# Kernel tuning notes

Measured on AMD Instinct MI355X. Metric: run time of the kernel, lower is better.

Reference implementation:

```python
import jax, jax.numpy as jnp
import numpy as np

B, C_IMG, H, W = 64, 256, 64, 64
HID, T = 512, 128
M, A = 128, 128  # multifeat_size, attfeat_size


def setup_inputs() -> dict:
    key = jax.random.key(0)
    ks = jax.random.split(key, 9)
    s = 0.02
    return {
        "img_feat": jax.random.normal(ks[0], (B, C_IMG, H, W), jnp.float32),
        "text_feat": jax.random.normal(ks[1], (B, HID, T), jnp.float32),
        "W_img": jax.random.normal(ks[2], (M, C_IMG), jnp.float32) * s,   # in_img_conv 1x1
        "W_txt": jax.random.normal(ks[3], (M, HID), jnp.float32) * s,     # in_text_conv 1d k=1
        "W_qfc": jax.random.normal(ks[4], (A, M), jnp.float32) * s,       # multi_qfc
        "W_ifc": jax.random.normal(ks[5], (A, M), jnp.float32) * s,       # multi_ifc
        "W_ipc": jax.random.normal(ks[6], (A, M), jnp.float32) * s,       # ifeat_proj_conv 1x1
        "W_qpc": jax.random.normal(ks[7], (A, M), jnp.float32) * s,       # qfeat_proj_conv 1x1
        "W_att": jax.random.normal(ks[8], (1, A), jnp.float32) * s,       # att_conv 1x1
    }


def reference(img_feat, text_feat, W_img, W_txt, W_qfc, W_ifc, W_ipc, W_qpc, W_att):
    b, c, h, w = img_feat.shape
    n = h * w  # conv_feat_num
    x = img_feat.reshape(b, c, n)
    # in_img_conv: dropout(id) -> 1x1 conv -> tanh ; in_text_conv analogous
    in_ifeat = jnp.tanh(jnp.einsum("mc,bcn->bmn", W_img, x))        # [B,M,HW]
    in_qfeat = jnp.tanh(jnp.einsum("mh,bht->bmt", W_txt, text_feat))  # [B,M,T]

    # text-guided image attention branch
    qfeatatt = jnp.mean(in_qfeat, axis=2) @ W_qfc.T                  # [B,A]
    ifeatproj = jnp.einsum("am,bmn->ban", W_ipc, in_ifeat)           # [B,A,HW]
    addfeat_i = jnp.tanh(qfeatatt[:, :, None] + ifeatproj)

    # image-guided text attention branch
    ifeatatt = jnp.mean(in_ifeat, axis=2) @ W_ifc.T                  # [B,A]
    qfeatproj = jnp.einsum("am,bmt->bat", W_qpc, in_qfeat)           # [B,A,T]
    addfeat_q = jnp.tanh(ifeatatt[:, :, None] + qfeatproj)

    attfeat_join = jnp.concatenate([addfeat_i, addfeat_q], axis=2)   # [B,A,HW+T]
    att_logits = jnp.einsum("a,ban->bn", W_att[0], attfeat_join)     # [B,HW+T]
    att = jax.nn.softmax(att_logits, axis=1)

    joint_feat = jnp.concatenate([in_ifeat, in_qfeat], axis=2)       # [B,M,HW+T]
    att_feat = jnp.einsum("bmn,bn->bm", joint_feat, att)             # [B,M]
    return att_feat, att
```

## Files before the change

### kernel.cpp

```cpp
#include <hip/hip_runtime.h>
#include <hip/hip_bf16.h>

#define DI static __device__ __forceinline__

typedef unsigned short u16;
typedef unsigned int   u32;
typedef __bf16 bf16_t;
typedef __bf16 bf16x8 __attribute__((ext_vector_type(8)));
typedef float  f32x4  __attribute__((ext_vector_type(4)));

union BF8 { ushort4 u4[2]; bf16x8 v; };

DI u16 f2bf(float f) { union { bf16_t b; u16 u; } c; c.b = (bf16_t)f; return c.u; }
DI float bf2f(u32 lo) { union { u32 u; float f; } c; c.u = lo << 16; return c.f; }
DI float fast_tanh(float x) { float e = __expf(2.0f * x); return 1.0f - 2.0f / (e + 1.0f); }

constexpr int NB   = 64;
constexpr int HW   = 4096;
constexpr int TT   = 128;
constexpr int NTOT = HW + TT;

constexpr size_t WS_WIMG  = 0;
constexpr size_t WS_WTXT  = WS_WIMG  + 128ull*256*2;
constexpr size_t WS_WIPC  = WS_WTXT  + 128ull*512*2;
constexpr size_t WS_WQPC  = WS_WIPC  + 128ull*128*2;
constexpr size_t WS_IFEAT = WS_WQPC  + 128ull*128*2;
constexpr size_t WS_QFEAT = WS_IFEAT + (size_t)NB*128*HW*2;
constexpr size_t WS_QFP   = WS_QFEAT + (size_t)NB*128*TT*2;
constexpr size_t WS_LOGIT = WS_QFP   + (size_t)NB*128*TT*4;
constexpr size_t WS_ISUM  = WS_LOGIT + (size_t)NB*NTOT*4;
constexpr size_t WS_QSUM  = WS_ISUM  + (size_t)NB*128*4;
constexpr size_t WS_QATT  = WS_QSUM  + (size_t)NB*128*4;

__global__ void k_zero(float* __restrict__ p, int n) {
    int i = blockIdx.x * 256 + threadIdx.x;
    if (i < n) p[i] = 0.0f;
}

__global__ void k_convert4(const float* __restrict__ s0, const float* __restrict__ s1,
                           const float* __restrict__ s2, const float* __restrict__ s3,
                           bf16_t* __restrict__ d0, bf16_t* __restrict__ d1,
                           bf16_t* __restrict__ d2, bf16_t* __restrict__ d3) {
    int i = blockIdx.x * 256 + threadIdx.x;
    if (i < 32768) { d0[i] = (bf16_t)s0[i]; return; }
    i -= 32768;
    if (i < 65536) { d1[i] = (bf16_t)s1[i]; return; }
    i -= 65536;
    if (i < 16384) { d2[i] = (bf16_t)s2[i]; return; }
    i -= 16384;
    d3[i] = (bf16_t)s3[i];
}

__global__ void k_qatt(const float* __restrict__ qsum, const float* __restrict__ Wqfc,
                       float* __restrict__ qatt) {
    int b = blockIdx.x, a = threadIdx.x;
    const float* qs = qsum + b * 128;
    const float* wr = Wqfc + a * 128;
    float s = 0.f;
    for (int m = 0; m < 128; ++m) s += qs[m] * wr[m];
    qatt[b * 128 + a] = s * (1.0f / 128.0f);
}

__global__ void k_textlogits(const float* __restrict__ isum, const float* __restrict__ Wifc,
                             const float* __restrict__ Watt, const float* __restrict__ qfp,
                             float* __restrict__ logits) {
    int b = blockIdx.x, tid = threadIdx.x;
    __shared__ float ia[128];
    __shared__ float wat[128];
    __shared__ float part[2][128];
    if (tid < 128) {
        float s = 0.f;
        const float* is = isum + b * 128;
        const float* wr = Wifc + tid * 128;
        for (int m = 0; m < 128; ++m) s += is[m] * wr[m];
        ia[tid]  = s * (1.0f / 4096.0f);
        wat[tid] = Watt[tid];
    }
    __syncthreads();
    int t = tid & 127, h = tid >> 7;
    const float* qp = qfp + ((size_t)b * 128 + h * 64) * 128 + t;
    float s = 0.f;
    for (int a0 = 0; a0 < 64; ++a0) {
        int a = h * 64 + a0;
        s += wat[a] * fast_tanh(ia[a] + qp[(size_t)a0 * 128]);
    }
    part[h][t] = s;
    __syncthreads();
    if (tid < 128) logits[b * NTOT + 4096 + tid] = part[0][tid] + part[1][tid];
}

__global__ void k_softmax(const float* __restrict__ logits, float* __restrict__ att) {
    int b = blockIdx.x, tid = threadIdx.x;
    const float* L = logits + (size_t)b * NTOT;
    float* O = att + (size_t)b * NTOT;
    __shared__ float red[4];
    __shared__ float red2[4];
    float mx = -3.0e38f;
    for (int i = tid; i < NTOT; i += 256) mx = fmaxf(mx, L[i]);
    for (int off = 1; off < 64; off <<= 1) mx = fmaxf(mx, __shfl_xor(mx, off, 64));
    if ((tid & 63) == 0) red[tid >> 6] = mx;
    __syncthreads();
    mx = fmaxf(fmaxf(red[0], red[1]), fmaxf(red[2], red[3]));
    float s = 0.f;
    for (int i = tid; i < NTOT; i += 256) {
        float e = __expf(L[i] - mx);
        O[i] = e;
        s += e;
    }
    for (int off = 1; off < 64; off <<= 1) s += __shfl_xor(s, off, 64);
    if ((tid & 63) == 0) red2[tid >> 6] = s;
    __syncthreads();
    float inv = 1.0f / (red2[0] + red2[1] + red2[2] + red2[3]);
    for (int i = tid; i < NTOT; i += 256) O[i] *= inv;
}

__global__ void k_attfeat(const bf16_t* __restrict__ ifeat, const bf16_t* __restrict__ qfeat,
                          const float* __restrict__ att, float* __restrict__ out) {
    int mg = blockIdx.x;
    int ns = blockIdx.y;
    int b  = blockIdx.z;
    int tid = threadIdx.x;
    const u16* F = (const u16*)ifeat + ((size_t)b * 128 + mg * 8) * HW;
    const u16* Q = (const u16*)qfeat + ((size_t)b * 128 + mg * 8) * TT;
    const float* A_ = att + (size_t)b * NTOT;
    float acc[8] = {0, 0, 0, 0, 0, 0, 0, 0};
    int i0 = ns * 512;
#pragma unroll
    for (int it = 0; it < 2; ++it) {
        int i = i0 + it * 256 + tid;
        float2 a2 = *(const float2*)&A_[2 * i];
#pragma unroll
        for (int r = 0; r < 8; ++r) {
            u32 pk = *(const u32*)&F[(size_t)r * HW + 2 * i];
            acc[r] += bf2f(pk & 0xffffu) * a2.x + bf2f(pk >> 16) * a2.y;
        }
    }
    if (ns == 0 && tid < TT / 2) {
        float2 a2 = *(const float2*)&A_[HW + 2 * tid];
#pragma unroll
        for (int r = 0; r < 8; ++r) {
            u32 pk = *(const u32*)&Q[(size_t)r * TT + 2 * tid];
            acc[r] += bf2f(pk & 0xffffu) * a2.x + bf2f(pk >> 16) * a2.y;
        }
    }
    __shared__ float red[4][8];
    int lane = tid & 63, wv = tid >> 6;
#pragma unroll
    for (int r = 0; r < 8; ++r) {
        float s = acc[r];
        s += __shfl_xor(s, 1, 64);
        s += __shfl_xor(s, 2, 64);
        s += __shfl_xor(s, 4, 64);
        s += __shfl_xor(s, 8, 64);
        s += __shfl_xor(s, 16, 64);
        s += __shfl_xor(s, 32, 64);
        if (lane == 0) red[wv][r] = s;
    }
    __syncthreads();
    if (tid < 8)
        atomicAdd(&out[(size_t)b * 128 + mg * 8 + tid],
                  red[0][tid] + red[1][tid] + red[2][tid] + red[3][tid]);
}

template <int C, bool IMG>
__global__ __launch_bounds__(256, 4) void k_chain(
    const float* __restrict__ xin, const bf16_t* __restrict__ Wa, const bf16_t* __restrict__ Wp,
    const float* __restrict__ qatt, const float* __restrict__ Watt, bf16_t* __restrict__ feat_out,
    float* __restrict__ sums, float* __restrict__ proj_out, int S) {
    constexpr int NCH = C / 128;
    __shared__ u16 XY[128 * 68];
    __shared__ u16 Y1[64 * 132];
    __shared__ float lred[4][64];
    __shared__ float qf_l[128];
    __shared__ float wa_l[128];

    const int tid = threadIdx.x;
    const int b  = blockIdx.y;
    const int n0 = blockIdx.x * 64;
    const int l  = tid & 63, w = tid >> 6;
    const int lr = l & 15, g = l >> 4;

    if constexpr (IMG) {
        if (tid < 128) {
            qf_l[tid] = qatt[b * 128 + tid];
            wa_l[tid] = Watt[tid];
        }
    }

    f32x4 acc1[2][4];
#pragma unroll
    for (int rt = 0; rt < 2; ++rt)
#pragma unroll
        for (int ct = 0; ct < 4; ++ct)
#pragma unroll
            for (int r = 0; r < 4; ++r) acc1[rt][ct][r] = 0.f;

    const bf16_t* wa0 = Wa + (size_t)(w * 32 + lr) * C + g * 8;
    const int colb = (tid & 15) * 4;
    const int r0   = tid >> 4;

    for (int h = 0; h < NCH; ++h) {
        {
            const float* xb = xin + (size_t)b * C * S + (size_t)h * 128 * S + n0 + colb;
#pragma unroll
            for (int p = 0; p < 8; ++p) {
                int c2 = p * 16 + r0;
                float4 f = *(const float4*)(xb + (size_t)c2 * S);
                u16 v[4] = {f2bf(f.x), f2bf(f.y), f2bf(f.z), f2bf(f.w)};
                int rot = c2 & 3;
#pragma unroll
                for (int s = 0; s < 4; ++s) {
                    int jj = (s + rot) & 3;
                    XY[(colb + jj) * 132 + c2] = v[jj];
                }
            }
        }
        __syncthreads();
#pragma unroll
        for (int ks2 = 0; ks2 < 4; ++ks2) {
            int ks = h * 4 + ks2;
            bf16x8 af0 = *(const bf16x8*)(wa0 + ks * 32);
            bf16x8 af1 = *(const bf16x8*)(wa0 + (size_t)16 * C + ks * 32);
#pragma unroll
            for (int ct = 0; ct < 4; ++ct) {
                BF8 bu;
                const u16* p = &XY[(ct * 16 + lr) * 132 + ks2 * 32 + g * 8];
                bu.u4[0] = *(const ushort4*)p;
                bu.u4[1] = *(const ushort4*)(p + 4);
                acc1[0][ct] = __builtin_amdgcn_mfma_f32_16x16x32_bf16(af0, bu.v, acc1[0][ct], 0, 0, 0);
                acc1[1][ct] = __builtin_amdgcn_mfma_f32_16x16x32_bf16(af1, bu.v, acc1[1][ct], 0, 0, 0);
            }
        }
        __syncthreads();
    }

    float y[2][4][4];
#pragma unroll
    for (int rt = 0; rt < 2; ++rt)
#pragma unroll
        for (int ct = 0; ct < 4; ++ct)
#pragma unroll
            for (int r = 0; r < 4; ++r) y[rt][ct][r] = fast_tanh(acc1[rt][ct][r]);

#pragma unroll
    for (int rt = 0; rt < 2; ++rt)
#pragma unroll
        for (int r = 0; r < 4; ++r) {
            float s = y[rt][0][r] + y[rt][1][r] + y[rt][2][r] + y[rt][3][r];
            s += __shfl_xor(s, 1, 64);
            s += __shfl_xor(s, 2, 64);
            s += __shfl_xor(s, 4, 64);
            s += __shfl_xor(s, 8, 64);
            if (lr == 0) atomicAdd(&sums[b * 128 + w * 32 + rt * 16 + g * 4 + r], s);
        }

#pragma unroll
    for (int rt = 0; rt < 2; ++rt)
#pragma unroll
        for (int ct = 0; ct < 4; ++ct) {
            int m0 = w * 32 + rt * 16 + g * 4;
            int c2 = ct * 16 + lr;
#pragma unroll
            for (int r = 0; r < 4; r += 2) {
                u32 pk = (u32)f2bf(y[rt][ct][r]) | ((u32)f2bf(y[rt][ct][r + 1]) << 16);
                *(u32*)&Y1[c2 * 132 + m0 + r] = pk;
            }
#pragma unroll
            for (int r = 0; r < 4; ++r) XY[(m0 + r) * 68 + c2] = f2bf(y[rt][ct][r]);
        }
    __syncthreads();

    f32x4 acc2[2][4];
#pragma unroll
    for (int rt = 0; rt < 2; ++rt)
#pragma unroll
        for (int ct = 0; ct < 4; ++ct)
#pragma unroll
            for (int r = 0; r < 4; ++r) acc2[rt][ct][r] = 0.f;

    const bf16_t* wp0 = Wp + (size_t)(w * 32 + lr) * 128 + g * 8;
#pragma unroll
    for (int ks = 0; ks < 4; ++ks) {
        bf16x8 af0 = *(const bf16x8*)(wp0 + ks * 32);
        bf16x8 af1 = *(const bf16x8*)(wp0 + 16 * 128 + ks * 32);
#pragma unroll
        for (int ct = 0; ct < 4; ++ct) {
            BF8 bu;
            const u16* p = &Y1[(ct * 16 + lr) * 132 + ks * 32 + g * 8];
            bu.u4[0] = *(const ushort4*)p;
            bu.u4[1] = *(const ushort4*)(p + 4);
            acc2[0][ct] = __builtin_amdgcn_mfma_f32_16x16x32_bf16(af0, bu.v, acc2[0][ct], 0, 0, 0);
            acc2[1][ct] = __builtin_amdgcn_mfma_f32_16x16x32_bf16(af1, bu.v, acc2[1][ct], 0, 0, 0);
        }
    }

    {
        u16* fb = (u16*)feat_out + (size_t)b * 128 * S + n0;
#pragma unroll
        for (int it = 0; it < 8; ++it) {
            int m = w * 32 + it * 4 + g;
            int nc = lr * 4;
            ushort4 v = *(const ushort4*)&XY[m * 68 + nc];
            *(ushort4*)(fb + (size_t)m * S + nc) = v;
        }
    }

    if constexpr (IMG) {
        float ps[4] = {0, 0, 0, 0};
#pragma unroll
        for (int rt = 0; rt < 2; ++rt)
#pragma unroll
            for (int r = 0; r < 4; ++r) {
                int a = w * 32 + rt * 16 + g * 4 + r;
                float qa = qf_l[a], wv = wa_l[a];
#pragma unroll
                for (int ct = 0; ct < 4; ++ct) ps[ct] += wv * fast_tanh(qa + acc2[rt][ct][r]);
            }
#pragma unroll
        for (int ct = 0; ct < 4; ++ct) {
            ps[ct] += __shfl_xor(ps[ct], 16, 64);
            ps[ct] += __shfl_xor(ps[ct], 32, 64);
        }
        if (g == 0) {
#pragma unroll
            for (int ct = 0; ct < 4; ++ct) lred[w][ct * 16 + lr] = ps[ct];
        }
        __syncthreads();
        if (tid < 64)
            proj_out[(size_t)b * NTOT + n0 + tid] =
                lred[0][tid] + lred[1][tid] + lred[2][tid] + lred[3][tid];
    } else {
#pragma unroll
        for (int rt = 0; rt < 2; ++rt)
#pragma unroll
            for (int ct = 0; ct < 4; ++ct) {
                int a = w * 32 + rt * 16 + g * 4;
                int t = n0 + ct * 16 + lr;
#pragma unroll
                for (int r = 0; r < 4; ++r)
                    proj_out[((size_t)b * 128 + a + r) * 128 + t] = acc2[rt][ct][r];
            }
    }
}

extern "C" void kernel_launch(void* const* d_in, const int* in_sizes, int n_in, void* d_out,
                              int out_size, void* d_ws, size_t ws_size, hipStream_t stream) {
    (void)in_sizes; (void)n_in; (void)out_size; (void)ws_size;
    const float* img  = (const float*)d_in[0];
    const float* txt  = (const float*)d_in[1];
    const float* Wimg = (const float*)d_in[2];
    const float* Wtxt = (const float*)d_in[3];
    const float* Wqfc = (const float*)d_in[4];
    const float* Wifc = (const float*)d_in[5];
    const float* Wipc = (const float*)d_in[6];
    const float* Wqpc = (const float*)d_in[7];
    const float* Watt = (const float*)d_in[8];

    char* ws = (char*)d_ws;
    bf16_t* wimg_b  = (bf16_t*)(ws + WS_WIMG);
    bf16_t* wtxt_b  = (bf16_t*)(ws + WS_WTXT);
    bf16_t* wipc_b  = (bf16_t*)(ws + WS_WIPC);
    bf16_t* wqpc_b  = (bf16_t*)(ws + WS_WQPC);
    bf16_t* ifeat_b = (bf16_t*)(ws + WS_IFEAT);
    bf16_t* qfeat_b = (bf16_t*)(ws + WS_QFEAT);
    float*  qfp     = (float*)(ws + WS_QFP);
    float*  logits  = (float*)(ws + WS_LOGIT);
    float*  isum    = (float*)(ws + WS_ISUM);
    float*  qsum    = (float*)(ws + WS_QSUM);
    float*  qatt    = (float*)(ws + WS_QATT);

    float* out_feat = (float*)d_out;
    float* out_att  = (float*)d_out + 64 * 128;

    k_zero<<<(2 * 64 * 128 + 255) / 256, 256, 0, stream>>>(isum, 2 * 64 * 128);
    k_zero<<<(64 * 128 + 255) / 256, 256, 0, stream>>>(out_feat, 64 * 128);

    k_convert4<<<131072 / 256, 256, 0, stream>>>(Wimg, Wtxt, Wipc, Wqpc,
                                                 wimg_b, wtxt_b, wipc_b, wqpc_b);

    k_chain<512, false><<<dim3(2, 64), 256, 0, stream>>>(txt, wtxt_b, wqpc_b, nullptr, nullptr,
                                                         qfeat_b, qsum, qfp, TT);
    k_qatt<<<64, 128, 0, stream>>>(qsum, Wqfc, qatt);
    k_chain<256, true><<<dim3(64, 64), 256, 0, stream>>>(img, wimg_b, wipc_b, qatt, Watt,
                                                         ifeat_b, isum, logits, HW);
    k_textlogits<<<64, 256, 0, stream>>>(isum, Wifc, Watt, qfp, logits);
    k_softmax<<<64, 256, 0, stream>>>(logits, out_att);
    k_attfeat<<<dim3(16, 4, 64), 256, 0, stream>>>(ifeat_b, qfeat_b, out_att, out_feat);
}
```

Baseline: 491.8 us.

## Fuse small kernels, double-buffer chain loads, vectorize attfeat reduction

Merges the zero and weight-convert launches into one init kernel. Folds the qatt matvec into the image chain kernel and combines text logits with the softmax in one kernel that keeps logits in shared memory. The chain kernel now prefetches 64-channel chunks into double-buffered LDS so global loads overlap the MFMA work. The attfeat kernel switches to 16-byte bf16 loads with four rows per half-block. Together these cut launch count and global round trips, at the cost of recomputing qatt in every image block.

```diff
diff --git a/kernel.cpp b/kernel.cpp
--- a/kernel.cpp
+++ b/kernel.cpp
@@ -28,90 +28,291 @@
 constexpr size_t WS_QFEAT = WS_IFEAT + (size_t)NB*128*HW*2;
 constexpr size_t WS_QFP   = WS_QFEAT + (size_t)NB*128*TT*2;
 constexpr size_t WS_LOGIT = WS_QFP   + (size_t)NB*128*TT*4;
-constexpr size_t WS_ISUM  = WS_LOGIT + (size_t)NB*NTOT*4;
+constexpr size_t WS_ISUM  = WS_LOGIT + (size_t)NB*HW*4;
 constexpr size_t WS_QSUM  = WS_ISUM  + (size_t)NB*128*4;
-constexpr size_t WS_QATT  = WS_QSUM  + (size_t)NB*128*4;
-
-__global__ void k_zero(float* __restrict__ p, int n) {
+
+__global__ void k_init(const float* __restrict__ s0, const float* __restrict__ s1,
+                       const float* __restrict__ s2, const float* __restrict__ s3,
+                       bf16_t* __restrict__ d0, bf16_t* __restrict__ d1,
+                       bf16_t* __restrict__ d2, bf16_t* __restrict__ d3,
+                       float* __restrict__ sums, float* __restrict__ outf) {
     int i = blockIdx.x * 256 + threadIdx.x;
-    if (i < n) p[i] = 0.0f;
+    if (i < 16384) sums[i] = 0.f;
+    else if (i < 24576) outf[i - 16384] = 0.f;
+    int j = i;
+    if (j < 32768) { d0[j] = (bf16_t)s0[j]; return; }
+    j -= 32768;
+    if (j < 65536) { d1[j] = (bf16_t)s1[j]; return; }
+    j -= 65536;
+    if (j < 16384) { d2[j] = (bf16_t)s2[j]; return; }
+    j -= 16384;
+    d3[j] = (bf16_t)s3[j];
 }
 
-__global__ void k_convert4(const float* __restrict__ s0, const float* __restrict__ s1,
-                           const float* __restrict__ s2, const float* __restrict__ s3,
-                           bf16_t* __restrict__ d0, bf16_t* __restrict__ d1,
-                           bf16_t* __restrict__ d2, bf16_t* __restrict__ d3) {
-    int i = blockIdx.x * 256 + threadIdx.x;
-    if (i < 32768) { d0[i] = (bf16_t)s0[i]; return; }
-    i -= 32768;
-    if (i < 65536) { d1[i] = (bf16_t)s1[i]; return; }
-    i -= 65536;
-    if (i < 16384) { d2[i] = (bf16_t)s2[i]; return; }
-    i -= 16384;
-    d3[i] = (bf16_t)s3[i];
+template <int C, bool IMG>
+__global__ __launch_bounds__(256, 4) void k_chain(
+    const float* __restrict__ xin, const bf16_t* __restrict__ Wa, const bf16_t* __restrict__ Wp,
+    const float* __restrict__ qsum, const float* __restrict__ Wqfc, const float* __restrict__ Watt,
+    bf16_t* __restrict__ feat_out, float* __restrict__ sums, float* __restrict__ proj_out, int S) {
+    constexpr int NCH = C / 64;
+    __shared__ u16 XY[2][64 * 68];
+    __shared__ u16 Y1[64 * 132];
+    __shared__ float lred[4][64];
+    __shared__ float qf_l[128];
+    __shared__ float wa_l[128];
+
+    const int tid = threadIdx.x;
+    const int b  = blockIdx.y;
+    const int n0 = blockIdx.x * 64;
+    const int l  = tid & 63, w = tid >> 6;
+    const int lr = l & 15, g = l >> 4;
+
+    f32x4 acc1[2][4];
+#pragma unroll
+    for (int rt = 0; rt < 2; ++rt)
+#pragma unroll
+        for (int ct = 0; ct < 4; ++ct)
+#pragma unroll
+            for (int r = 0; r < 4; ++r) acc1[rt][ct][r] = 0.f;
+
+    const bf16_t* wa0 = Wa + (size_t)(w * 32 + lr) * C + g * 8;
+    const int colb = (tid & 15) * 4;
+    const int rb   = tid >> 4;
+    const float* xbase = xin + (size_t)b * C * S + n0 + colb;
+    float4 pf[4];
+
+#pragma unroll
+    for (int p = 0; p < 4; ++p) pf[p] = *(const float4*)(xbase + (size_t)(rb + p * 16) * S);
+#pragma unroll
+    for (int p = 0; p < 4; ++p) {
+        int c2 = rb + p * 16;
+        u16 v[4] = {f2bf(pf[p].x), f2bf(pf[p].y), f2bf(pf[p].z), f2bf(pf[p].w)};
+        int rot = c2 & 3;
+#pragma unroll
+        for (int s = 0; s < 4; ++s) { int jj = (s + rot) & 3; XY[0][(colb + jj) * 68 + c2] = v[jj]; }
+    }
+
+    for (int h = 0; h < NCH; ++h) {
+        __syncthreads();
+        if (h + 1 < NCH) {
+            const float* xb = xbase + (size_t)((h + 1) * 64) * S;
+#pragma unroll
+            for (int p = 0; p < 4; ++p) pf[p] = *(const float4*)(xb + (size_t)(rb + p * 16) * S);
+        }
+#pragma unroll
+        for (int ks2 = 0; ks2 < 2; ++ks2) {
+            int ks = h * 2 + ks2;
+            bf16x8 af0 = *(const bf16x8*)(wa0 + ks * 32);
+            bf16x8 af1 = *(const bf16x8*)(wa0 + (size_t)16 * C + ks * 32);
+#pragma unroll
+            for (int ct = 0; ct < 4; ++ct) {
+                BF8 bu;
+                const u16* p = &XY[h & 1][(ct * 16 + lr) * 68 + ks2 * 32 + g * 8];
+                bu.u4[0] = *(const ushort4*)p;
+                bu.u4[1] = *(const ushort4*)(p + 4);
+                acc1[0][ct] = __builtin_amdgcn_mfma_f32_16x16x32_bf16(af0, bu.v, acc1[0][ct], 0, 0, 0);
+                acc1[1][ct] = __builtin_amdgcn_mfma_f32_16x16x32_bf16(af1, bu.v, acc1[1][ct], 0, 0, 0);
+            }
+        }
+        if (h + 1 < NCH) {
+#pragma unroll
+            for (int p = 0; p < 4; ++p) {
+                int c2 = rb + p * 16;
+                u16 v[4] = {f2bf(pf[p].x), f2bf(pf[p].y), f2bf(pf[p].z), f2bf(pf[p].w)};
+                int rot = c2 & 3;
+#pragma unroll
+                for (int s = 0; s < 4; ++s) {
+                    int jj = (s + rot) & 3;
+                    XY[(h + 1) & 1][(colb + jj) * 68 + c2] = v[jj];
+                }
+            }
+        }
+    }
+    __syncthreads();
+
+#pragma unroll
+    for (int rt = 0; rt < 2; ++rt)
+#pragma unroll
+        for (int ct = 0; ct < 4; ++ct)
+#pragma unroll
+            for (int r = 0; r < 4; ++r) acc1[rt][ct][r] = fast_tanh(acc1[rt][ct][r]);
+
+#pragma unroll
+    for (int rt = 0; rt < 2; ++rt)
+#pragma unroll
+        for (int r = 0; r < 4; ++r) {
+            float s = acc1[rt][0][r] + acc1[rt][1][r] + acc1[rt][2][r] + acc1[rt][3][r];
+            s += __shfl_xor(s, 1, 64);
+            s += __shfl_xor(s, 2, 64);
+            s += __shfl_xor(s, 4, 64);
+            s += __shfl_xor(s, 8, 64);
+            if (lr == 0) atomicAdd(&sums[b * 128 + w * 32 + rt * 16 + g * 4 + r], s);
+        }
+
+    u16* Y1N = &XY[0][0];
+#pragma unroll
+    for (int rt = 0; rt < 2; ++rt)
+#pragma unroll
+        for (int ct = 0; ct < 4; ++ct) {
+            int m0 = w * 32 + rt * 16 + g * 4;
+            int c2 = ct * 16 + lr;
+#pragma unroll
+            for (int r = 0; r < 4; r += 2) {
+                u32 pk = (u32)f2bf(acc1[rt][ct][r]) | ((u32)f2bf(acc1[rt][ct][r + 1]) << 16);
+                *(u32*)&Y1[c2 * 132 + m0 + r] = pk;
+            }
+#pragma unroll
+            for (int r = 0; r < 4; ++r) Y1N[(m0 + r) * 68 + c2] = f2bf(acc1[rt][ct][r]);
+        }
+    __syncthreads();
+
+    if constexpr (IMG) {
+        if (tid < 128) {
+            const float4* qs4 = (const float4*)(qsum + b * 128);
+            const float4* wr4 = (const float4*)(Wqfc + (size_t)tid * 128);
+            float s = 0.f;
+#pragma unroll 8
+            for (int m = 0; m < 32; ++m) {
+                float4 a = qs4[m], c = wr4[m];
+                s += a.x * c.x + a.y * c.y + a.z * c.z + a.w * c.w;
+            }
+            qf_l[tid] = s * (1.0f / 128.0f);
+            wa_l[tid] = Watt[tid];
+        }
+    }
+
+    f32x4 acc2[2][4];
+#pragma unroll
+    for (int rt = 0; rt < 2; ++rt)
+#pragma unroll
+        for (int ct = 0; ct < 4; ++ct)
+#pragma unroll
+            for (int r = 0; r < 4; ++r) acc2[rt][ct][r] = 0.f;
+
+    const bf16_t* wp0 = Wp + (size_t)(w * 32 + lr) * 128 + g * 8;
+#pragma unroll
+    for (int ks = 0; ks < 4; ++ks) {
+        bf16x8 af0 = *(const bf16x8*)(wp0 + ks * 32);
+        bf16x8 af1 = *(const bf16x8*)(wp0 + 16 * 128 + ks * 32);
+#pragma unroll
+        for (int ct = 0; ct < 4; ++ct) {
+            BF8 bu;
+            const u16* p = &Y1[(ct * 16 + lr) * 132 + ks * 32 + g * 8];
+            bu.u4[0] = *(const ushort4*)p;
+            bu.u4[1] = *(const ushort4*)(p + 4);
+            acc2[0][ct] = __builtin_amdgcn_mfma_f32_16x16x32_bf16(af0, bu.v, acc2[0][ct], 0, 0, 0);
+            acc2[1][ct] = __builtin_amdgcn_mfma_f32_16x16x32_bf16(af1, bu.v, acc2[1][ct], 0, 0, 0);
+        }
+    }
+
+    {
+        u16* fb = (u16*)feat_out + (size_t)b * 128 * S + n0;
+#pragma unroll
+        for (int it = 0; it < 8; ++it) {
+            int m = w * 32 + it * 4 + g;
+            int nc = lr * 4;
+            ushort4 v = *(const ushort4*)&Y1N[m * 68 + nc];
+            *(ushort4*)(fb + (size_t)m * S + nc) = v;
+        }
+    }
+
+    if constexpr (IMG) {
+        __syncthreads();
+        float ps[4] = {0, 0, 0, 0};
+#pragma unroll
+        for (int rt = 0; rt < 2; ++rt)
+#pragma unroll
+            for (int r = 0; r < 4; ++r) {
+                int a = w * 32 + rt * 16 + g * 4 + r;
+                float qa = qf_l[a], wv = wa_l[a];
+#pragma unroll
+                for (int ct = 0; ct < 4; ++ct) ps[ct] += wv * fast_tanh(qa + acc2[rt][ct][r]);
+            }
+#pragma unroll
+        for (int ct = 0; ct < 4; ++ct) {
+            ps[ct] += __shfl_xor(ps[ct], 16, 64);
+            ps[ct] += __shfl_xor(ps[ct], 32, 64);
+        }
+        if (g == 0) {
+#pragma unroll
+            for (int ct = 0; ct < 4; ++ct) lred[w][ct * 16 + lr] = ps[ct];
+        }
+        __syncthreads();
+        if (tid < 64)
+            proj_out[(size_t)b * HW + n0 + tid] =
+                lred[0][tid] + lred[1][tid] + lred[2][tid] + lred[3][tid];
+    } else {
+#pragma unroll
+        for (int rt = 0; rt < 2; ++rt)
+#pragma unroll
+            for (int ct = 0; ct < 4; ++ct) {
+                int a = w * 32 + rt * 16 + g * 4;
+                int t = n0 + ct * 16 + lr;
+#pragma unroll
+                for (int r = 0; r < 4; ++r)
+                    proj_out[((size_t)b * 128 + a + r) * 128 + t] = acc2[rt][ct][r];
+            }
+    }
 }
 
-__global__ void k_qatt(const float* __restrict__ qsum, const float* __restrict__ Wqfc,
-                       float* __restrict__ qatt) {
-    int b = blockIdx.x, a = threadIdx.x;
-    const float* qs = qsum + b * 128;
-    const float* wr = Wqfc + a * 128;
-    float s = 0.f;
-    for (int m = 0; m < 128; ++m) s += qs[m] * wr[m];
-    qatt[b * 128 + a] = s * (1.0f / 128.0f);
-}
-
-__global__ void k_textlogits(const float* __restrict__ isum, const float* __restrict__ Wifc,
-                             const float* __restrict__ Watt, const float* __restrict__ qfp,
-                             float* __restrict__ logits) {
+__global__ void k_finish(const float* __restrict__ isum, const float* __restrict__ Wifc,
+                         const float* __restrict__ Watt, const float* __restrict__ qfp,
+                         const float* __restrict__ logitsI, float* __restrict__ att) {
     int b = blockIdx.x, tid = threadIdx.x;
+    __shared__ float L[NTOT];
     __shared__ float ia[128];
     __shared__ float wat[128];
     __shared__ float part[2][128];
+    __shared__ float redm[4];
+    __shared__ float reds[4];
+
     if (tid < 128) {
+        const float4* is4 = (const float4*)(isum + b * 128);
+        const float4* wr4 = (const float4*)(Wifc + (size_t)tid * 128);
         float s = 0.f;
-        const float* is = isum + b * 128;
-        const float* wr = Wifc + tid * 128;
-        for (int m = 0; m < 128; ++m) s += is[m] * wr[m];
+#pragma unroll 8
+        for (int m = 0; m < 32; ++m) {
+            float4 a = is4[m], c = wr4[m];
+            s += a.x * c.x + a.y * c.y + a.z * c.z + a.w * c.w;
+        }
         ia[tid]  = s * (1.0f / 4096.0f);
         wat[tid] = Watt[tid];
     }
-    __syncthreads();
-    int t = tid & 127, h = tid >> 7;
-    const float* qp = qfp + ((size_t)b * 128 + h * 64) * 128 + t;
-    float s = 0.f;
-    for (int a0 = 0; a0 < 64; ++a0) {
-        int a = h * 64 + a0;
-        s += wat[a] * fast_tanh(ia[a] + qp[(size_t)a0 * 128]);
-    }
-    part[h][t] = s;
-    __syncthreads();
-    if (tid < 128) logits[b * NTOT + 4096 + tid] = part[0][tid] + part[1][tid];
-}
-
-__global__ void k_softmax(const float* __restrict__ logits, float* __restrict__ att) {
-    int b = blockIdx.x, tid = threadIdx.x;
-    const float* L = logits + (size_t)b * NTOT;
+    const float4* LI = (const float4*)(logitsI + (size_t)b * HW);
+#pragma unroll
+    for (int i = 0; i < 4; ++i) *(float4*)&L[(i * 256 + tid) * 4] = LI[i * 256 + tid];
+    __syncthreads();
+
+    {
+        int t = tid & 127, h = tid >> 7;
+        const float* qp = qfp + ((size_t)b * 128 + h * 64) * 128 + t;
+        float s = 0.f;
+        for (int a0 = 0; a0 < 64; ++a0)
+            s += wat[h * 64 + a0] * fast_tanh(ia[h * 64 + a0] + qp[(size_t)a0 * 128]);
+        part[h][t] = s;
+    }
+    __syncthreads();
+    if (tid < 128) L[HW + tid] = part[0][tid] + part[1][tid];
+    __syncthreads();
+
     float* O = att + (size_t)b * NTOT;
-    __shared__ float red[4];
-    __shared__ float red2[4];
     float mx = -3.0e38f;
     for (int i = tid; i < NTOT; i += 256) mx = fmaxf(mx, L[i]);
     for (int off = 1; off < 64; off <<= 1) mx = fmaxf(mx, __shfl_xor(mx, off, 64));
-    if ((tid & 63) == 0) red[tid >> 6] = mx;
-    __syncthreads();
-    mx = fmaxf(fmaxf(red[0], red[1]), fmaxf(red[2], red[3]));
+    if ((tid & 63) == 0) redm[tid >> 6] = mx;
+    __syncthreads();
+    mx = fmaxf(fmaxf(redm[0], redm[1]), fmaxf(redm[2], redm[3]));
     float s = 0.f;
     for (int i = tid; i < NTOT; i += 256) {
         float e = __expf(L[i] - mx);
-        O[i] = e;
+        L[i] = e;
         s += e;
     }
     for (int off = 1; off < 64; off <<= 1) s += __shfl_xor(s, off, 64);
-    if ((tid & 63) == 0) red2[tid >> 6] = s;
-    __syncthreads();
-    float inv = 1.0f / (red2[0] + red2[1] + red2[2] + red2[3]);
-    for (int i = tid; i < NTOT; i += 256) O[i] *= inv;
+    if ((tid & 63) == 0) reds[tid >> 6] = s;
+    __syncthreads();
+    float inv = 1.0f / (reds[0] + reds[1] + reds[2] + reds[3]);
+    for (int i = tid; i < NTOT; i += 256) O[i] = L[i] * inv;
 }
 
 __global__ void k_attfeat(const bf16_t* __restrict__ ifeat, const bf16_t* __restrict__ qfeat,
@@ -120,33 +321,48 @@
     int ns = blockIdx.y;
     int b  = blockIdx.z;
     int tid = threadIdx.x;
-    const u16* F = (const u16*)ifeat + ((size_t)b * 128 + mg * 8) * HW;
-    const u16* Q = (const u16*)qfeat + ((size_t)b * 128 + mg * 8) * TT;
+    int half = tid >> 7;
+    int q = tid & 127;
+    int cx = q * 8;
     const float* A_ = att + (size_t)b * NTOT;
-    float acc[8] = {0, 0, 0, 0, 0, 0, 0, 0};
-    int i0 = ns * 512;
-#pragma unroll
-    for (int it = 0; it < 2; ++it) {
-        int i = i0 + it * 256 + tid;
-        float2 a2 = *(const float2*)&A_[2 * i];
-#pragma unroll
-        for (int r = 0; r < 8; ++r) {
-            u32 pk = *(const u32*)&F[(size_t)r * HW + 2 * i];
-            acc[r] += bf2f(pk & 0xffffu) * a2.x + bf2f(pk >> 16) * a2.y;
-        }
-    }
-    if (ns == 0 && tid < TT / 2) {
-        float2 a2 = *(const float2*)&A_[HW + 2 * tid];
-#pragma unroll
-        for (int r = 0; r < 8; ++r) {
-            u32 pk = *(const u32*)&Q[(size_t)r * TT + 2 * tid];
-            acc[r] += bf2f(pk & 0xffffu) * a2.x + bf2f(pk >> 16) * a2.y;
-        }
-    }
-    __shared__ float red[4][8];
+    const u16* F = (const u16*)ifeat + ((size_t)b * 128 + mg * 8 + half * 4) * HW + ns * 1024 + cx;
+
+    float a8[8];
+    {
+        float4 a0 = *(const float4*)&A_[ns * 1024 + cx];
+        float4 a1 = *(const float4*)&A_[ns * 1024 + cx + 4];
+        a8[0] = a0.x; a8[1] = a0.y; a8[2] = a0.z; a8[3] = a0.w;
+        a8[4] = a1.x; a8[5] = a1.y; a8[6] = a1.z; a8[7] = a1.w;
+    }
+    float acc[4] = {0, 0, 0, 0};
+#pragma unroll
+    for (int r = 0; r < 4; ++r) {
+        uint4 pk = *(const uint4*)&F[(size_t)r * HW];
+        acc[r] += bf2f(pk.x & 0xffffu) * a8[0] + bf2f(pk.x >> 16) * a8[1]
+                + bf2f(pk.y & 0xffffu) * a8[2] + bf2f(pk.y >> 16) * a8[3]
+                + bf2f(pk.z & 0xffffu) * a8[4] + bf2f(pk.z >> 16) * a8[5]
+                + bf2f(pk.w & 0xffffu) * a8[6] + bf2f(pk.w >> 16) * a8[7];
+    }
+    if (ns == 0 && q < 16) {
+        const u16* Q = (const u16*)qfeat + ((size_t)b * 128 + mg * 8 + half * 4) * TT + cx;
+        float b8[8];
+        float4 a0 = *(const float4*)&A_[HW + cx];
+        float4 a1 = *(const float4*)&A_[HW + cx + 4];
+        b8[0] = a0.x; b8[1] = a0.y; b8[2] = a0.z; b8[3] = a0.w;
+        b8[4] = a1.x; b8[5] = a1.y; b8[6] = a1.z; b8[7] = a1.w;
+#pragma unroll
+        for (int r = 0; r < 4; ++r) {
+            uint4 pk = *(const uint4*)&Q[(size_t)r * TT];
+            acc[r] += bf2f(pk.x & 0xffffu) * b8[0] + bf2f(pk.x >> 16) * b8[1]
+                    + bf2f(pk.y & 0xffffu) * b8[2] + bf2f(pk.y >> 16) * b8[3]
+                    + bf2f(pk.z & 0xffffu) * b8[4] + bf2f(pk.z >> 16) * b8[5]
+                    + bf2f(pk.w & 0xffffu) * b8[6] + bf2f(pk.w >> 16) * b8[7];
+        }
+    }
+    __shared__ float red[4][4];
     int lane = tid & 63, wv = tid >> 6;
 #pragma unroll
-    for (int r = 0; r < 8; ++r) {
+    for (int r = 0; r < 4; ++r) {
         float s = acc[r];
         s += __shfl_xor(s, 1, 64);
         s += __shfl_xor(s, 2, 64);
@@ -157,189 +373,10 @@
         if (lane == 0) red[wv][r] = s;
     }
     __syncthreads();
-    if (tid < 8)
-        atomicAdd(&out[(size_t)b * 128 + mg * 8 + tid],
-                  red[0][tid] + red[1][tid] + red[2][tid] + red[3][tid]);
-}
-
-template <int C, bool IMG>
-__global__ __launch_bounds__(256, 4) void k_chain(
-    const float* __restrict__ xin, const bf16_t* __restrict__ Wa, const bf16_t* __restrict__ Wp,
-    const float* __restrict__ qatt, const float* __restrict__ Watt, bf16_t* __restrict__ feat_out,
-    float* __restrict__ sums, float* __restrict__ proj_out, int S) {
-    constexpr int NCH = C / 128;
-    __shared__ u16 XY[128 * 68];
-    __shared__ u16 Y1[64 * 132];
-    __shared__ float lred[4][64];
-    __shared__ float qf_l[128];
-    __shared__ float wa_l[128];
-
-    const int tid = threadIdx.x;
-    const int b  = blockIdx.y;
-    const int n0 = blockIdx.x * 64;
-    const int l  = tid & 63, w = tid >> 6;
-    const int lr = l & 15, g = l >> 4;
-
-    if constexpr (IMG) {
-        if (tid < 128) {
-            qf_l[tid] = qatt[b * 128 + tid];
-            wa_l[tid] = Watt[tid];
-        }
-    }
-
-    f32x4 acc1[2][4];
-#pragma unroll
-    for (int rt = 0; rt < 2; ++rt)
-#pragma unroll
-        for (int ct = 0; ct < 4; ++ct)
-#pragma unroll
-            for (int r = 0; r < 4; ++r) acc1[rt][ct][r] = 0.f;
-
-    const bf16_t* wa0 = Wa + (size_t)(w * 32 + lr) * C + g * 8;
-    const int colb = (tid & 15) * 4;
-    const int r0   = tid >> 4;
-
-    for (int h = 0; h < NCH; ++h) {
-        {
-            const float* xb = xin + (size_t)b * C * S + (size_t)h * 128 * S + n0 + colb;
-#pragma unroll
-            for (int p = 0; p < 8; ++p) {
-                int c2 = p * 16 + r0;
-                float4 f = *(const float4*)(xb + (size_t)c2 * S);
-                u16 v[4] = {f2bf(f.x), f2bf(f.y), f2bf(f.z), f2bf(f.w)};
-                int rot = c2 & 3;
-#pragma unroll
-                for (int s = 0; s < 4; ++s) {
-                    int jj = (s + rot) & 3;
-                    XY[(colb + jj) * 132 + c2] = v[jj];
-                }
-            }
-        }
-        __syncthreads();
-#pragma unroll
-        for (int ks2 = 0; ks2 < 4; ++ks2) {
-            int ks = h * 4 + ks2;
-            bf16x8 af0 = *(const bf16x8*)(wa0 + ks * 32);
-            bf16x8 af1 = *(const bf16x8*)(wa0 + (size_t)16 * C + ks * 32);
-#pragma unroll
-            for (int ct = 0; ct < 4; ++ct) {
-                BF8 bu;
-                const u16* p = &XY[(ct * 16 + lr) * 132 + ks2 * 32 + g * 8];
-                bu.u4[0] = *(const ushort4*)p;
-                bu.u4[1] = *(const ushort4*)(p + 4);
-                acc1[0][ct] = __builtin_amdgcn_mfma_f32_16x16x32_bf16(af0, bu.v, acc1[0][ct], 0, 0, 0);
-                acc1[1][ct] = __builtin_amdgcn_mfma_f32_16x16x32_bf16(af1, bu.v, acc1[1][ct], 0, 0, 0);
-            }
-        }
-        __syncthreads();
-    }
-
-    float y[2][4][4];
-#pragma unroll
-    for (int rt = 0; rt < 2; ++rt)
-#pragma unroll
-        for (int ct = 0; ct < 4; ++ct)
-#pragma unroll
-            for (int r = 0; r < 4; ++r) y[rt][ct][r] = fast_tanh(acc1[rt][ct][r]);
-
-#pragma unroll
-    for (int rt = 0; rt < 2; ++rt)
-#pragma unroll
-        for (int r = 0; r < 4; ++r) {
-            float s = y[rt][0][r] + y[rt][1][r] + y[rt][2][r] + y[rt][3][r];
-            s += __shfl_xor(s, 1, 64);
-            s += __shfl_xor(s, 2, 64);
-            s += __shfl_xor(s, 4, 64);
-            s += __shfl_xor(s, 8, 64);
-            if (lr == 0) atomicAdd(&sums[b * 128 + w * 32 + rt * 16 + g * 4 + r], s);
-        }
-
-#pragma unroll
-    for (int rt = 0; rt < 2; ++rt)
-#pragma unroll
-        for (int ct = 0; ct < 4; ++ct) {
-            int m0 = w * 32 + rt * 16 + g * 4;
-            int c2 = ct * 16 + lr;
-#pragma unroll
-            for (int r = 0; r < 4; r += 2) {
-                u32 pk = (u32)f2bf(y[rt][ct][r]) | ((u32)f2bf(y[rt][ct][r + 1]) << 16);
-                *(u32*)&Y1[c2 * 132 + m0 + r] = pk;
-            }
-#pragma unroll
-            for (int r = 0; r < 4; ++r) XY[(m0 + r) * 68 + c2] = f2bf(y[rt][ct][r]);
-        }
-    __syncthreads();
-
-    f32x4 acc2[2][4];
-#pragma unroll
-    for (int rt = 0; rt < 2; ++rt)
-#pragma unroll
-        for (int ct = 0; ct < 4; ++ct)
-#pragma unroll
-            for (int r = 0; r < 4; ++r) acc2[rt][ct][r] = 0.f;
-
-    const bf16_t* wp0 = Wp + (size_t)(w * 32 + lr) * 128 + g * 8;
-#pragma unroll
-    for (int ks = 0; ks < 4; ++ks) {
-        bf16x8 af0 = *(const bf16x8*)(wp0 + ks * 32);
-        bf16x8 af1 = *(const bf16x8*)(wp0 + 16 * 128 + ks * 32);
-#pragma unroll
-        for (int ct = 0; ct < 4; ++ct) {
-            BF8 bu;
-            const u16* p = &Y1[(ct * 16 + lr) * 132 + ks * 32 + g * 8];
-            bu.u4[0] = *(const ushort4*)p;
-            bu.u4[1] = *(const ushort4*)(p + 4);
-            acc2[0][ct] = __builtin_amdgcn_mfma_f32_16x16x32_bf16(af0, bu.v, acc2[0][ct], 0, 0, 0);
-            acc2[1][ct] = __builtin_amdgcn_mfma_f32_16x16x32_bf16(af1, bu.v, acc2[1][ct], 0, 0, 0);
-        }
-    }
-
-    {
-        u16* fb = (u16*)feat_out + (size_t)b * 128 * S + n0;
-#pragma unroll
-        for (int it = 0; it < 8; ++it) {
-            int m = w * 32 + it * 4 + g;
-            int nc = lr * 4;
-            ushort4 v = *(const ushort4*)&XY[m * 68 + nc];
-            *(ushort4*)(fb + (size_t)m * S + nc) = v;
-        }
-    }
-
-    if constexpr (IMG) {
-        float ps[4] = {0, 0, 0, 0};
-#pragma unroll
-        for (int rt = 0; rt < 2; ++rt)
-#pragma unroll
-            for (int r = 0; r < 4; ++r) {
-                int a = w * 32 + rt * 16 + g * 4 + r;
-                float qa = qf_l[a], wv = wa_l[a];
-#pragma unroll
-                for (int ct = 0; ct < 4; ++ct) ps[ct] += wv * fast_tanh(qa + acc2[rt][ct][r]);
-            }
-#pragma unroll
-        for (int ct = 0; ct < 4; ++ct) {
-            ps[ct] += __shfl_xor(ps[ct], 16, 64);
-            ps[ct] += __shfl_xor(ps[ct], 32, 64);
-        }
-        if (g == 0) {
-#pragma unroll
-            for (int ct = 0; ct < 4; ++ct) lred[w][ct * 16 + lr] = ps[ct];
-        }
-        __syncthreads();
-        if (tid < 64)
-            proj_out[(size_t)b * NTOT + n0 + tid] =
-                lred[0][tid] + lred[1][tid] + lred[2][tid] + lred[3][tid];
-    } else {
-#pragma unroll
-        for (int rt = 0; rt < 2; ++rt)
-#pragma unroll
-            for (int ct = 0; ct < 4; ++ct) {
-                int a = w * 32 + rt * 16 + g * 4;
-                int t = n0 + ct * 16 + lr;
-#pragma unroll
-                for (int r = 0; r < 4; ++r)
-                    proj_out[((size_t)b * 128 + a + r) * 128 + t] = acc2[rt][ct][r];
-            }
+    if (tid < 8) {
+        int rr = tid & 3, hh = tid >> 2;
+        atomicAdd(&out[(size_t)b * 128 + mg * 8 + hh * 4 + rr],
+                  red[2 * hh][rr] + red[2 * hh + 1][rr]);
     }
 }
 
@@ -367,23 +404,16 @@
     float*  logits  = (float*)(ws + WS_LOGIT);
     float*  isum    = (float*)(ws + WS_ISUM);
     float*  qsum    = (float*)(ws + WS_QSUM);
-    float*  qatt    = (float*)(ws + WS_QATT);
 
     float* out_feat = (float*)d_out;
     float* out_att  = (float*)d_out + 64 * 128;
 
-    k_zero<<<(2 * 64 * 128 + 255) / 256, 256, 0, stream>>>(isum, 2 * 64 * 128);
-    k_zero<<<(64 * 128 + 255) / 256, 256, 0, stream>>>(out_feat, 64 * 128);
-
-    k_convert4<<<131072 / 256, 256, 0, stream>>>(Wimg, Wtxt, Wipc, Wqpc,
-                                                 wimg_b, wtxt_b, wipc_b, wqpc_b);
-
+    k_init<<<131072 / 256, 256, 0, stream>>>(Wimg, Wtxt, Wipc, Wqpc, wimg_b, wtxt_b, wipc_b,
+                                             wqpc_b, isum, out_feat);
     k_chain<512, false><<<dim3(2, 64), 256, 0, stream>>>(txt, wtxt_b, wqpc_b, nullptr, nullptr,
-                                                         qfeat_b, qsum, qfp, TT);
-    k_qatt<<<64, 128, 0, stream>>>(qsum, Wqfc, qatt);
-    k_chain<256, true><<<dim3(64, 64), 256, 0, stream>>>(img, wimg_b, wipc_b, qatt, Watt,
+                                                         nullptr, qfeat_b, qsum, qfp, TT);
+    k_chain<256, true><<<dim3(64, 64), 256, 0, stream>>>(img, wimg_b, wipc_b, qsum, Wqfc, Watt,
                                                          ifeat_b, isum, logits, HW);
-    k_textlogits<<<64, 256, 0, stream>>>(isum, Wifc, Watt, qfp, logits);
-    k_softmax<<<64, 256, 0, stream>>>(logits, out_att);
+    k_finish<<<64, 256, 0, stream>>>(isum, Wifc, Watt, qfp, logits, out_att);
     k_attfeat<<<dim3(16, 4, 64), 256, 0, stream>>>(ifeat_b, qfeat_b, out_att, out_feat);
 }
```

After: 485.3 us. No clear change (-1.3%).
